# Kernel tuning notes

Measured on AMD Instinct MI355X. Metric: run time of the kernel, lower is better.

## Reference

```python
import jax, jax.numpy as jnp
import numpy as np

B, LT, LI, DT, DI, D, H = 128, 96, 64, 1024, 2048, 1024, 4
NEG = -2.0 ** 31  # tf.pow(-2.0, 31)
EPS = 1e-3        # keras LayerNormalization default epsilon


def _mha(q_in, k_in, v_in, q_mask, k_mask, Wq, Wk, Wv, Wo):
    # tf split-heads: chunk i of axis 2 -> head i; reshape (B,L,H,d) matches.
    d = D // H
    b = q_in.shape[0]
    q = (q_in @ Wq).reshape(b, -1, H, d)
    k = (k_in @ Wk).reshape(b, -1, H, d)
    v = (v_in @ Wv).reshape(b, -1, H, d)
    scores = jnp.einsum('bqhd,bkhd->bhqk', q, k) / jnp.sqrt(jnp.float32(d))
    mask = (q_mask != 0)[:, None, :, None] & (k_mask != 0)[:, None, None, :]  # [B,1,Lq,Lk]
    scores = jnp.where(mask, scores, NEG)
    attn = jax.nn.softmax(scores, axis=-1)
    attn = jnp.where(mask, attn, 0.0)  # dropout rate is 0.0 -> identity
    out = jnp.einsum('bhqk,bkhd->bqhd', attn, v).reshape(b, -1, D)
    return out @ Wo


def _ln(x, g, b):
    m = jnp.mean(x, axis=-1, keepdims=True)
    v = jnp.var(x, axis=-1, keepdims=True)
    return (x - m) / jnp.sqrt(v + EPS) * g + b


def setup_inputs() -> dict:
    key = jax.random.key(0)
    ks = iter(jax.random.split(key, 40))
    s = 0.02
    inp = {
        'text_embedding': jax.random.normal(next(ks), (B, LT, DT), jnp.float32),
        'image_embedding': jax.random.normal(next(ks), (B, LI, DI), jnp.float32),
        'text_mask': jax.random.randint(next(ks), (B, LT), 0, 2, jnp.int32),
        'image_mask': jax.random.randint(next(ks), (B, LI), 0, 2, jnp.int32),
        'W_tp': jax.random.normal(next(ks), (DT, D), jnp.float32) * s,
        'b_tp': jnp.zeros((D,), jnp.float32),
        'W_ip': jax.random.normal(next(ks), (DI, D), jnp.float32) * s,
        'b_ip': jnp.zeros((D,), jnp.float32),
        # text cross-attn (query=image_proj, key=text_proj, value=RAW text)
        'ta_Wq': jax.random.normal(next(ks), (D, D), jnp.float32) * s,
        'ta_Wk': jax.random.normal(next(ks), (D, D), jnp.float32) * s,
        'ta_Wv': jax.random.normal(next(ks), (DT, D), jnp.float32) * s,
        'ta_Wo': jax.random.normal(next(ks), (D, D), jnp.float32) * s,
        # image cross-attn (query=text_proj, key=image_proj, value=RAW image)
        'ia_Wq': jax.random.normal(next(ks), (D, D), jnp.float32) * s,
        'ia_Wk': jax.random.normal(next(ks), (D, D), jnp.float32) * s,
        'ia_Wv': jax.random.normal(next(ks), (DI, D), jnp.float32) * s,
        'ia_Wo': jax.random.normal(next(ks), (D, D), jnp.float32) * s,
        # self-attention blocks
        'ts_Wq': jax.random.normal(next(ks), (D, D), jnp.float32) * s,
        'ts_Wk': jax.random.normal(next(ks), (D, D), jnp.float32) * s,
        'ts_Wv': jax.random.normal(next(ks), (D, D), jnp.float32) * s,
        'ts_Wo': jax.random.normal(next(ks), (D, D), jnp.float32) * s,
        'is_Wq': jax.random.normal(next(ks), (D, D), jnp.float32) * s,
        'is_Wk': jax.random.normal(next(ks), (D, D), jnp.float32) * s,
        'is_Wv': jax.random.normal(next(ks), (D, D), jnp.float32) * s,
        'is_Wo': jax.random.normal(next(ks), (D, D), jnp.float32) * s,
        # layernorm params
        'ln_ta_g': jnp.ones((D,), jnp.float32), 'ln_ta_b': jnp.zeros((D,), jnp.float32),
        'ln_ia_g': jnp.ones((D,), jnp.float32), 'ln_ia_b': jnp.zeros((D,), jnp.float32),
        'ln_ts_g': jnp.ones((D,), jnp.float32), 'ln_ts_b': jnp.zeros((D,), jnp.float32),
        'ln_is_g': jnp.ones((D,), jnp.float32), 'ln_is_b': jnp.zeros((D,), jnp.float32),
    }
    return inp


def reference(text_embedding, image_embedding, text_mask, image_mask,
              W_tp, b_tp, W_ip, b_ip,
              ta_Wq, ta_Wk, ta_Wv, ta_Wo,
              ia_Wq, ia_Wk, ia_Wv, ia_Wo,
              ts_Wq, ts_Wk, ts_Wv, ts_Wo,
              is_Wq, is_Wk, is_Wv, is_Wo,
              ln_ta_g, ln_ta_b, ln_ia_g, ln_ia_b,
              ln_ts_g, ln_ts_b, ln_is_g, ln_is_b):
    text_proj = text_embedding @ W_tp + b_tp    # [B,LT,D]
    image_proj = image_embedding @ W_ip + b_ip  # [B,LI,D]
    # cross attention (note asymmetric query/key masks, raw-value inputs)
    text_att = _mha(image_proj, text_proj, text_embedding, image_mask, text_mask,
                    ta_Wq, ta_Wk, ta_Wv, ta_Wo)   # [B,LI,D]
    image_att = _mha(text_proj, image_proj, image_embedding, text_mask, image_mask,
                     ia_Wq, ia_Wk, ia_Wv, ia_Wo)  # [B,LT,D]
    text_att = _ln(text_att, ln_ta_g, ln_ta_b)
    image_att = _ln(image_att, ln_ia_g, ln_ia_b)
    # self attention
    text_att = _mha(text_att, text_att, text_att, image_mask, image_mask,
                    ts_Wq, ts_Wk, ts_Wv, ts_Wo)
    image_att = _mha(image_att, image_att, image_att, text_mask, text_mask,
                     is_Wq, is_Wk, is_Wv, is_Wo)
    text_att = _ln(text_att, ln_ts_g, ln_ts_b)
    image_att = _ln(image_att, ln_is_g, ln_is_b)
    return (text_att, image_att)
```

## Files before the change

### kernel.cpp

```cpp
#include <hip/hip_runtime.h>

typedef __bf16 bf16_t;
typedef __attribute__((ext_vector_type(8))) __bf16 bf16x8;
typedef __attribute__((ext_vector_type(4))) __bf16 bf16x4;
typedef __attribute__((ext_vector_type(4))) float f32x4;

__device__ __forceinline__ void async_copy16(const bf16_t* g, bf16_t* l) {
    __builtin_amdgcn_global_load_lds(
        (const __attribute__((address_space(1))) void*)g,
        (__attribute__((address_space(3))) void*)l, 16, 0, 0);
}

__global__ __launch_bounds__(256) void transpose_to_bf16(const float* __restrict__ in,
                                                         bf16_t* __restrict__ out,
                                                         int K, int N) {
    __shared__ float tile[32][33];
    int t = threadIdx.x;
    int tx = t & 31, ty = t >> 5;
    int n0 = blockIdx.x * 32, k0 = blockIdx.y * 32;
#pragma unroll
    for (int i = 0; i < 4; i++) {
        int k = k0 + ty + i * 8;
        tile[ty + i * 8][tx] = in[(size_t)k * N + n0 + tx];
    }
    __syncthreads();
#pragma unroll
    for (int i = 0; i < 4; i++) {
        int n = n0 + ty + i * 8;
        out[(size_t)n * K + k0 + tx] = (bf16_t)tile[tx][ty + i * 8];
    }
}

__global__ __launch_bounds__(256) void gemm_bt(const bf16_t* __restrict__ A,
                                               const bf16_t* __restrict__ Bt,
                                               const float* __restrict__ bias,
                                               float* __restrict__ outF,
                                               bf16_t* __restrict__ outB,
                                               int M, int N, int K) {
    __shared__ bf16_t As[128 * 32];
    __shared__ bf16_t Bs[128 * 32];
    const int t = threadIdx.x;
    const int w = t >> 6, lane = t & 63;
    const int quad = lane >> 4, l16 = lane & 15;
    const int bm = blockIdx.x * 128, bn = blockIdx.y * 128;
    const int wm = (w >> 1) * 64, wn = (w & 1) * 64;

    const f32x4 zero = {0.f, 0.f, 0.f, 0.f};
    f32x4 acc[4][4];
#pragma unroll
    for (int i = 0; i < 4; i++)
#pragma unroll
        for (int j = 0; j < 4; j++) acc[i][j] = zero;

    const int srow = t >> 2;
    const int scol = (t & 3) * 8;
    const bf16_t* ga = A + (size_t)(bm + srow) * K + scol;
    const bf16_t* gb = Bt + (size_t)(bn + srow) * K + scol;
    bf16_t* la = As + w * 512;
    bf16_t* lb = Bs + w * 512;

    for (int k0 = 0; k0 < K; k0 += 32) {
        async_copy16(ga + k0, la);
        async_copy16(ga + k0 + (size_t)64 * K, la + 2048);
        async_copy16(gb + k0, lb);
        async_copy16(gb + k0 + (size_t)64 * K, lb + 2048);
        __syncthreads();
        bf16x8 af[4], bf[4];
#pragma unroll
        for (int i = 0; i < 4; i++)
            af[i] = *(const bf16x8*)(As + (wm + i * 16 + l16) * 32 + quad * 8);
#pragma unroll
        for (int j = 0; j < 4; j++)
            bf[j] = *(const bf16x8*)(Bs + (wn + j * 16 + l16) * 32 + quad * 8);
#pragma unroll
        for (int i = 0; i < 4; i++)
#pragma unroll
            for (int j = 0; j < 4; j++)
                acc[i][j] = __builtin_amdgcn_mfma_f32_16x16x32_bf16(af[i], bf[j], acc[i][j], 0, 0, 0);
        __syncthreads();
    }

#pragma unroll
    for (int i = 0; i < 4; i++) {
        int r0 = bm + wm + i * 16 + quad * 4;
#pragma unroll
        for (int j = 0; j < 4; j++) {
            int c = bn + wn + j * 16 + l16;
            float bsv = bias ? bias[c] : 0.f;
#pragma unroll
            for (int r = 0; r < 4; r++) {
                float v = acc[i][j][r] + bsv;
                size_t idx = (size_t)(r0 + r) * N + c;
                if (outF) outF[idx] = v;
                if (outB) outB[idx] = (bf16_t)v;
            }
        }
    }
}

__global__ __launch_bounds__(256) void gemm_f32a(const float* __restrict__ A,
                                                 const bf16_t* __restrict__ Bt,
                                                 const float* __restrict__ bias,
                                                 bf16_t* __restrict__ outB,
                                                 int M, int N, int K) {
    __shared__ bf16_t As[128 * 32];
    __shared__ bf16_t Bs[128 * 32];
    const int t = threadIdx.x;
    const int w = t >> 6, lane = t & 63;
    const int quad = lane >> 4, l16 = lane & 15;
    const int bm = blockIdx.x * 128, bn = blockIdx.y * 128;
    const int wm = (w >> 1) * 64, wn = (w & 1) * 64;

    const f32x4 zero = {0.f, 0.f, 0.f, 0.f};
    f32x4 acc[4][4];
#pragma unroll
    for (int i = 0; i < 4; i++)
#pragma unroll
        for (int j = 0; j < 4; j++) acc[i][j] = zero;

    const int arow = t >> 1, acol = (t & 1) * 16;
    const float* ga = A + (size_t)(bm + arow) * K + acol;
    const int srow = t >> 2, scol = (t & 3) * 8;
    const bf16_t* gb = Bt + (size_t)(bn + srow) * K + scol;
    bf16_t* lb = Bs + w * 512;

    for (int k0 = 0; k0 < K; k0 += 32) {
        async_copy16(gb + k0, lb);
        async_copy16(gb + k0 + (size_t)64 * K, lb + 2048);
        float4 v0 = *(const float4*)(ga + k0);
        float4 v1 = *(const float4*)(ga + k0 + 4);
        float4 v2 = *(const float4*)(ga + k0 + 8);
        float4 v3 = *(const float4*)(ga + k0 + 12);
        bf16x8 o0, o1;
        o0[0] = (__bf16)v0.x; o0[1] = (__bf16)v0.y; o0[2] = (__bf16)v0.z; o0[3] = (__bf16)v0.w;
        o0[4] = (__bf16)v1.x; o0[5] = (__bf16)v1.y; o0[6] = (__bf16)v1.z; o0[7] = (__bf16)v1.w;
        o1[0] = (__bf16)v2.x; o1[1] = (__bf16)v2.y; o1[2] = (__bf16)v2.z; o1[3] = (__bf16)v2.w;
        o1[4] = (__bf16)v3.x; o1[5] = (__bf16)v3.y; o1[6] = (__bf16)v3.z; o1[7] = (__bf16)v3.w;
        *(bf16x8*)(As + arow * 32 + acol) = o0;
        *(bf16x8*)(As + arow * 32 + acol + 8) = o1;
        __syncthreads();
        bf16x8 af[4], bf[4];
#pragma unroll
        for (int i = 0; i < 4; i++)
            af[i] = *(const bf16x8*)(As + (wm + i * 16 + l16) * 32 + quad * 8);
#pragma unroll
        for (int j = 0; j < 4; j++)
            bf[j] = *(const bf16x8*)(Bs + (wn + j * 16 + l16) * 32 + quad * 8);
#pragma unroll
        for (int i = 0; i < 4; i++)
#pragma unroll
            for (int j = 0; j < 4; j++)
                acc[i][j] = __builtin_amdgcn_mfma_f32_16x16x32_bf16(af[i], bf[j], acc[i][j], 0, 0, 0);
        __syncthreads();
    }

#pragma unroll
    for (int i = 0; i < 4; i++) {
        int r0 = bm + wm + i * 16 + quad * 4;
#pragma unroll
        for (int j = 0; j < 4; j++) {
            int c = bn + wn + j * 16 + l16;
            float bsv = bias ? bias[c] : 0.f;
#pragma unroll
            for (int r = 0; r < 4; r++)
                outB[(size_t)(r0 + r) * N + c] = (bf16_t)(acc[i][j][r] + bsv);
        }
    }
}

template <int LQ, int LK>
__global__ __launch_bounds__(256) void attn_kernel(const bf16_t* __restrict__ Q,
                                                   const bf16_t* __restrict__ Kb,
                                                   const bf16_t* __restrict__ V,
                                                   const int* __restrict__ qmask,
                                                   const int* __restrict__ kmask,
                                                   bf16_t* __restrict__ O) {
    constexpr int VSTR = LK + 8;
    constexpr int NQT = LQ / 16, NKT = LK / 16, NKB = LK / 32;
    __shared__ bf16_t Vt[256 * VSTR];
    __shared__ bf16_t Pb[4 * 16 * LK];

    const int t = threadIdx.x;
    const int w = t >> 6, lane = t & 63;
    const int quad = lane >> 4, l16 = lane & 15;
    const int b = blockIdx.x >> 2;
    const int h = blockIdx.x & 3;
    const int hoff = h * 256;

    for (int idx = t; idx < LK * 32; idx += 256) {
        int k = idx % LK;
        int e0 = (idx / LK) * 8;
        bf16x8 v = *(const bf16x8*)(V + (size_t)(b * LK + k) * 1024 + hoff + e0);
#pragma unroll
        for (int j = 0; j < 8; j++) Vt[(e0 + j) * VSTR + k] = v[j];
    }
    __syncthreads();

    bf16_t* P = Pb + w * (16 * LK);

    for (int qt = w; qt < NQT; qt += 4) {
        const int qrow = b * LQ + qt * 16;
        bf16x8 qf[8];
#pragma unroll
        for (int kb = 0; kb < 8; kb++)
            qf[kb] = *(const bf16x8*)(Q + (size_t)(qrow + l16) * 1024 + hoff + kb * 32 + quad * 8);

        f32x4 s[NKT];
        const f32x4 zero = {0.f, 0.f, 0.f, 0.f};
#pragma unroll
        for (int nt = 0; nt < NKT; nt++) {
            f32x4 a = zero;
#pragma unroll
            for (int kb = 0; kb < 8; kb++) {
                bf16x8 kf = *(const bf16x8*)(Kb + (size_t)(b * LK + nt * 16 + l16) * 1024 + hoff + kb * 32 + quad * 8);
                a = __builtin_amdgcn_mfma_f32_16x16x32_bf16(qf[kb], kf, a, 0, 0, 0);
            }
            s[nt] = a;
        }

        int km[NKT];
#pragma unroll
        for (int nt = 0; nt < NKT; nt++) km[nt] = kmask[b * LK + nt * 16 + l16];
        int qmv[4];
#pragma unroll
        for (int r = 0; r < 4; r++) qmv[r] = qmask[b * LQ + qt * 16 + quad * 4 + r];

        float rmax[4], rsum[4];
#pragma unroll
        for (int r = 0; r < 4; r++) rmax[r] = -3.0e38f;
#pragma unroll
        for (int nt = 0; nt < NKT; nt++)
#pragma unroll
            for (int r = 0; r < 4; r++) {
                float v = s[nt][r] * 0.0625f;
                bool ok = (qmv[r] != 0) && (km[nt] != 0);
                s[nt][r] = ok ? v : -3.0e38f;
                rmax[r] = fmaxf(rmax[r], s[nt][r]);
            }
#pragma unroll
        for (int r = 0; r < 4; r++)
            for (int off = 1; off < 16; off <<= 1)
                rmax[r] = fmaxf(rmax[r], __shfl_xor(rmax[r], off, 16));
#pragma unroll
        for (int r = 0; r < 4; r++) rsum[r] = 0.f;
#pragma unroll
        for (int nt = 0; nt < NKT; nt++)
#pragma unroll
            for (int r = 0; r < 4; r++) {
                float p = (s[nt][r] > -1.0e38f) ? __expf(s[nt][r] - rmax[r]) : 0.f;
                s[nt][r] = p;
                rsum[r] += p;
            }
#pragma unroll
        for (int r = 0; r < 4; r++)
            for (int off = 1; off < 16; off <<= 1)
                rsum[r] += __shfl_xor(rsum[r], off, 16);
#pragma unroll
        for (int r = 0; r < 4; r++) rsum[r] = (rsum[r] > 0.f) ? 1.f / rsum[r] : 0.f;

#pragma unroll
        for (int nt = 0; nt < NKT; nt++)
#pragma unroll
            for (int r = 0; r < 4; r++)
                P[(quad * 4 + r) * LK + nt * 16 + l16] = (bf16_t)(s[nt][r] * rsum[r]);
        asm volatile("s_waitcnt lgkmcnt(0)" ::: "memory");

        bf16x8 pf[NKB];
#pragma unroll
        for (int kb = 0; kb < NKB; kb++)
            pf[kb] = *(const bf16x8*)(P + l16 * LK + kb * 32 + quad * 8);

#pragma unroll
        for (int et = 0; et < 16; et++) {
            f32x4 o = zero;
#pragma unroll
            for (int kb = 0; kb < NKB; kb++) {
                bf16x8 vf = *(const bf16x8*)(Vt + (et * 16 + l16) * VSTR + kb * 32 + quad * 8);
                o = __builtin_amdgcn_mfma_f32_16x16x32_bf16(pf[kb], vf, o, 0, 0, 0);
            }
#pragma unroll
            for (int r = 0; r < 4; r++)
                O[(size_t)(qrow + quad * 4 + r) * 1024 + hoff + et * 16 + l16] = (bf16_t)o[r];
        }
    }
}

__global__ __launch_bounds__(256) void ln_kernel(const float* __restrict__ in,
                                                 const float* __restrict__ g,
                                                 const float* __restrict__ be,
                                                 float* __restrict__ outF,
                                                 bf16_t* __restrict__ outB) {
    __shared__ float red[8];
    const int row = blockIdx.x, t = threadIdx.x;
    const float* x = in + (size_t)row * 1024;
    float4 v = *(const float4*)(x + t * 4);
    float s = v.x + v.y + v.z + v.w;
    float ss = v.x * v.x + v.y * v.y + v.z * v.z + v.w * v.w;
    for (int off = 1; off < 64; off <<= 1) {
        s += __shfl_xor(s, off);
        ss += __shfl_xor(ss, off);
    }
    int w = t >> 6, lane = t & 63;
    if (lane == 0) { red[w * 2] = s; red[w * 2 + 1] = ss; }
    __syncthreads();
    if (t == 0) {
        float a = 0.f, b2 = 0.f;
        for (int i = 0; i < 4; i++) { a += red[i * 2]; b2 += red[i * 2 + 1]; }
        red[0] = a; red[1] = b2;
    }
    __syncthreads();
    float mean = red[0] * (1.f / 1024.f);
    float var = red[1] * (1.f / 1024.f) - mean * mean;
    float rstd = rsqrtf(var + 1e-3f);
    float4 gv = *(const float4*)(g + t * 4);
    float4 bv = *(const float4*)(be + t * 4);
    float y0 = (v.x - mean) * rstd * gv.x + bv.x;
    float y1 = (v.y - mean) * rstd * gv.y + bv.y;
    float y2 = (v.z - mean) * rstd * gv.z + bv.z;
    float y3 = (v.w - mean) * rstd * gv.w + bv.w;
    if (outF) {
        float4 o = {y0, y1, y2, y3};
        *(float4*)(outF + (size_t)row * 1024 + t * 4) = o;
    }
    if (outB) {
        bf16x4 o;
        o[0] = (__bf16)y0; o[1] = (__bf16)y1; o[2] = (__bf16)y2; o[3] = (__bf16)y3;
        *(bf16x4*)(outB + (size_t)row * 1024 + t * 4) = o;
    }
}

extern "C" void kernel_launch(void* const* d_in, const int* in_sizes, int n_in,
                              void* d_out, int out_size, void* d_ws, size_t ws_size,
                              hipStream_t stream) {
    (void)in_sizes; (void)n_in; (void)out_size; (void)ws_size;
    const float* tE = (const float*)d_in[0];
    const float* iE = (const float*)d_in[1];
    const int* tMask = (const int*)d_in[2];
    const int* iMask = (const int*)d_in[3];

    char* ws = (char*)d_ws;
    const size_t SLOT = (size_t)12288 * 1024 * 2;
    bf16_t* S[6];
    for (int i = 0; i < 6; i++) S[i] = (bf16_t*)(ws + i * SLOT);
    bf16_t* Wb = (bf16_t*)(ws + 6 * SLOT);
    float* f32_01 = (float*)S[0];
    float* f32_23 = (float*)S[2];

    auto TW = [&](int idx) {
        int K = (idx == 6 || idx == 14) ? 2048 : 1024;
        transpose_to_bf16<<<dim3(32, K / 32), 256, 0, stream>>>((const float*)d_in[idx], Wb, K, 1024);
    };
    auto gemm = [&](const bf16_t* A, const float* bias, float* oF, bf16_t* oB, int M, int K) {
        gemm_bt<<<dim3(M / 128, 8), 256, 0, stream>>>(A, Wb, bias, oF, oB, M, 1024, K);
    };
    auto gemmF = [&](const float* A, const float* bias, bf16_t* oB, int M, int K) {
        gemm_f32a<<<dim3(M / 128, 8), 256, 0, stream>>>(A, Wb, bias, oB, M, 1024, K);
    };

    TW(4);  gemmF(tE, (const float*)d_in[5], S[0], 12288, 1024);
    TW(6);  gemmF(iE, (const float*)d_in[7], S[1], 8192, 2048);
    TW(8);  gemm(S[1], nullptr, nullptr, S[2], 8192, 1024);
    TW(9);  gemm(S[0], nullptr, nullptr, S[3], 12288, 1024);
    TW(10); gemmF(tE, nullptr, S[4], 12288, 1024);
    attn_kernel<64, 96><<<512, 256, 0, stream>>>(S[2], S[3], S[4], iMask, tMask, S[5]);
    TW(12); gemm(S[0], nullptr, nullptr, S[2], 12288, 1024);
    TW(13); gemm(S[1], nullptr, nullptr, S[3], 8192, 1024);
    TW(14); gemmF(iE, nullptr, S[4], 8192, 2048);
    attn_kernel<96, 64><<<512, 256, 0, stream>>>(S[2], S[3], S[4], tMask, iMask, S[0]);
    TW(11); gemm(S[5], nullptr, f32_23, nullptr, 8192, 1024);
    ln_kernel<<<8192, 256, 0, stream>>>(f32_23, (const float*)d_in[24], (const float*)d_in[25], nullptr, S[1]);
    TW(15); gemm(S[0], nullptr, f32_23, nullptr, 12288, 1024);
    ln_kernel<<<12288, 256, 0, stream>>>(f32_23, (const float*)d_in[26], (const float*)d_in[27], nullptr, S[4]);
    TW(16); gemm(S[1], nullptr, nullptr, S[0], 8192, 1024);
    TW(17); gemm(S[1], nullptr, nullptr, S[2], 8192, 1024);
    TW(18); gemm(S[1], nullptr, nullptr, S[3], 8192, 1024);
    attn_kernel<64, 64><<<512, 256, 0, stream>>>(S[0], S[2], S[3], iMask, iMask, S[5]);
    TW(19); gemm(S[5], nullptr, f32_01, nullptr, 8192, 1024);
    ln_kernel<<<8192, 256, 0, stream>>>(f32_01, (const float*)d_in[28], (const float*)d_in[29], (float*)d_out, nullptr);
    TW(20); gemm(S[4], nullptr, nullptr, S[2], 12288, 1024);
    TW(21); gemm(S[4], nullptr, nullptr, S[3], 12288, 1024);
    TW(22); gemm(S[4], nullptr, nullptr, S[5], 12288, 1024);
    attn_kernel<96, 96><<<512, 256, 0, stream>>>(S[2], S[3], S[5], tMask, tMask, S[0]);
    TW(23); gemm(S[0], nullptr, f32_23, nullptr, 12288, 1024);
    ln_kernel<<<12288, 256, 0, stream>>>(f32_23, (const float*)d_in[30], (const float*)d_in[31],
                                         (float*)d_out + 8388608, nullptr);
}
```

Baseline: 1.184 ms.

## Batch projection GEMMs sharing an input into wide multi-output launches

Projections that read the same activation are merged into one GEMM with a wider N, via grouped weight transposes and a multi-pointer epilogue. This covers text proj with its value projection, image proj with its value projection, the Q/K pairs and the fused self-attention QKV. The f32-input GEMM now loads A with a row-strided pattern into padded LDS to reduce bank conflicts. Output-projection results are written as bf16 instead of f32, which halves LN input traffic but adds rounding before the layer norm. The intent is fewer launches, better GPU fill, and fewer passes over the shared activations.

Measured after the change: 1.076 ms. 9.1% less time.

```diff
diff --git a/kernel.cpp b/kernel.cpp
--- a/kernel.cpp
+++ b/kernel.cpp
@@ -11,9 +11,15 @@
         (__attribute__((address_space(3))) void*)l, 16, 0, 0);
 }
 
-__global__ __launch_bounds__(256) void transpose_to_bf16(const float* __restrict__ in,
-                                                         bf16_t* __restrict__ out,
-                                                         int K, int N) {
+__global__ __launch_bounds__(256) void transpose_group(const float* __restrict__ s0,
+                                                       const float* __restrict__ s1,
+                                                       const float* __restrict__ s2,
+                                                       bf16_t* __restrict__ dst, int K) {
+    const float* in;
+    if (blockIdx.z == 0) in = s0;
+    else if (blockIdx.z == 1) in = s1;
+    else in = s2;
+    bf16_t* out = dst + (size_t)blockIdx.z * 1024 * K;
     __shared__ float tile[32][33];
     int t = threadIdx.x;
     int tx = t & 31, ty = t >> 5;
@@ -21,7 +27,7 @@
 #pragma unroll
     for (int i = 0; i < 4; i++) {
         int k = k0 + ty + i * 8;
-        tile[ty + i * 8][tx] = in[(size_t)k * N + n0 + tx];
+        tile[ty + i * 8][tx] = in[(size_t)k * 1024 + n0 + tx];
     }
     __syncthreads();
 #pragma unroll
@@ -31,11 +37,18 @@
     }
 }
 
+__global__ __launch_bounds__(256) void fuse_bias(const float* __restrict__ src,
+                                                 float* __restrict__ out) {
+    int i = blockIdx.x * 256 + threadIdx.x;
+    out[i] = (i < 1024) ? src[i] : 0.f;
+}
+
 __global__ __launch_bounds__(256) void gemm_bt(const bf16_t* __restrict__ A,
                                                const bf16_t* __restrict__ Bt,
                                                const float* __restrict__ bias,
-                                               float* __restrict__ outF,
-                                               bf16_t* __restrict__ outB,
+                                               bf16_t* __restrict__ o0,
+                                               bf16_t* __restrict__ o1,
+                                               bf16_t* __restrict__ o2,
                                                int M, int N, int K) {
     __shared__ bf16_t As[128 * 32];
     __shared__ bf16_t Bs[128 * 32];
@@ -80,20 +93,22 @@
         __syncthreads();
     }
 
+    bf16_t* out;
+    if (bn < 1024) out = o0;
+    else if (bn < 2048) out = o1;
+    else out = o2;
+    const int cb = bn & 1023;
+    const int bbase = bn - cb;
 #pragma unroll
     for (int i = 0; i < 4; i++) {
         int r0 = bm + wm + i * 16 + quad * 4;
 #pragma unroll
         for (int j = 0; j < 4; j++) {
-            int c = bn + wn + j * 16 + l16;
-            float bsv = bias ? bias[c] : 0.f;
-#pragma unroll
-            for (int r = 0; r < 4; r++) {
-                float v = acc[i][j][r] + bsv;
-                size_t idx = (size_t)(r0 + r) * N + c;
-                if (outF) outF[idx] = v;
-                if (outB) outB[idx] = (bf16_t)v;
-            }
+            int c = cb + wn + j * 16 + l16;
+            float bsv = bias ? bias[bbase + c] : 0.f;
+#pragma unroll
+            for (int r = 0; r < 4; r++)
+                out[(size_t)(r0 + r) * 1024 + c] = (bf16_t)(acc[i][j][r] + bsv);
         }
     }
 }
@@ -101,9 +116,11 @@
 __global__ __launch_bounds__(256) void gemm_f32a(const float* __restrict__ A,
                                                  const bf16_t* __restrict__ Bt,
                                                  const float* __restrict__ bias,
-                                                 bf16_t* __restrict__ outB,
+                                                 bf16_t* __restrict__ o0,
+                                                 bf16_t* __restrict__ o1,
                                                  int M, int N, int K) {
-    __shared__ bf16_t As[128 * 32];
+    constexpr int ASTR = 40;
+    __shared__ bf16_t As[128 * ASTR];
     __shared__ bf16_t Bs[128 * 32];
     const int t = threadIdx.x;
     const int w = t >> 6, lane = t & 63;
@@ -118,8 +135,8 @@
 #pragma unroll
         for (int j = 0; j < 4; j++) acc[i][j] = zero;
 
-    const int arow = t >> 1, acol = (t & 1) * 16;
-    const float* ga = A + (size_t)(bm + arow) * K + acol;
+    const int arow = t >> 3, ac4 = (t & 7) * 4;
+    const float* ga = A + (size_t)(bm + arow) * K + ac4;
     const int srow = t >> 2, scol = (t & 3) * 8;
     const bf16_t* gb = Bt + (size_t)(bn + srow) * K + scol;
     bf16_t* lb = Bs + w * 512;
@@ -127,22 +144,22 @@
     for (int k0 = 0; k0 < K; k0 += 32) {
         async_copy16(gb + k0, lb);
         async_copy16(gb + k0 + (size_t)64 * K, lb + 2048);
-        float4 v0 = *(const float4*)(ga + k0);
-        float4 v1 = *(const float4*)(ga + k0 + 4);
-        float4 v2 = *(const float4*)(ga + k0 + 8);
-        float4 v3 = *(const float4*)(ga + k0 + 12);
-        bf16x8 o0, o1;
-        o0[0] = (__bf16)v0.x; o0[1] = (__bf16)v0.y; o0[2] = (__bf16)v0.z; o0[3] = (__bf16)v0.w;
-        o0[4] = (__bf16)v1.x; o0[5] = (__bf16)v1.y; o0[6] = (__bf16)v1.z; o0[7] = (__bf16)v1.w;
-        o1[0] = (__bf16)v2.x; o1[1] = (__bf16)v2.y; o1[2] = (__bf16)v2.z; o1[3] = (__bf16)v2.w;
-        o1[4] = (__bf16)v3.x; o1[5] = (__bf16)v3.y; o1[6] = (__bf16)v3.z; o1[7] = (__bf16)v3.w;
-        *(bf16x8*)(As + arow * 32 + acol) = o0;
-        *(bf16x8*)(As + arow * 32 + acol + 8) = o1;
+        float4 av[4];
+#pragma unroll
+        for (int i = 0; i < 4; i++)
+            av[i] = *(const float4*)(ga + (size_t)i * 32 * K + k0);
+#pragma unroll
+        for (int i = 0; i < 4; i++) {
+            bf16x4 c;
+            c[0] = (__bf16)av[i].x; c[1] = (__bf16)av[i].y;
+            c[2] = (__bf16)av[i].z; c[3] = (__bf16)av[i].w;
+            *(bf16x4*)(As + (arow + i * 32) * ASTR + ac4) = c;
+        }
         __syncthreads();
         bf16x8 af[4], bf[4];
 #pragma unroll
         for (int i = 0; i < 4; i++)
-            af[i] = *(const bf16x8*)(As + (wm + i * 16 + l16) * 32 + quad * 8);
+            af[i] = *(const bf16x8*)(As + (wm + i * 16 + l16) * ASTR + quad * 8);
 #pragma unroll
         for (int j = 0; j < 4; j++)
             bf[j] = *(const bf16x8*)(Bs + (wn + j * 16 + l16) * 32 + quad * 8);
@@ -154,16 +171,19 @@
         __syncthreads();
     }
 
+    bf16_t* out = (bn < 1024) ? o0 : o1;
+    const int cb = bn & 1023;
+    const int bbase = bn - cb;
 #pragma unroll
     for (int i = 0; i < 4; i++) {
         int r0 = bm + wm + i * 16 + quad * 4;
 #pragma unroll
         for (int j = 0; j < 4; j++) {
-            int c = bn + wn + j * 16 + l16;
-            float bsv = bias ? bias[c] : 0.f;
+            int c = cb + wn + j * 16 + l16;
+            float bsv = bias ? bias[bbase + c] : 0.f;
 #pragma unroll
             for (int r = 0; r < 4; r++)
-                outB[(size_t)(r0 + r) * N + c] = (bf16_t)(acc[i][j][r] + bsv);
+                out[(size_t)(r0 + r) * 1024 + c] = (bf16_t)(acc[i][j][r] + bsv);
         }
     }
 }
@@ -285,17 +305,17 @@
     }
 }
 
-__global__ __launch_bounds__(256) void ln_kernel(const float* __restrict__ in,
+__global__ __launch_bounds__(256) void ln_kernel(const bf16_t* __restrict__ in,
                                                  const float* __restrict__ g,
                                                  const float* __restrict__ be,
                                                  float* __restrict__ outF,
                                                  bf16_t* __restrict__ outB) {
     __shared__ float red[8];
     const int row = blockIdx.x, t = threadIdx.x;
-    const float* x = in + (size_t)row * 1024;
-    float4 v = *(const float4*)(x + t * 4);
-    float s = v.x + v.y + v.z + v.w;
-    float ss = v.x * v.x + v.y * v.y + v.z * v.z + v.w * v.w;
+    bf16x4 xb = *(const bf16x4*)(in + (size_t)row * 1024 + t * 4);
+    float x0 = (float)xb[0], x1 = (float)xb[1], x2 = (float)xb[2], x3 = (float)xb[3];
+    float s = x0 + x1 + x2 + x3;
+    float ss = x0 * x0 + x1 * x1 + x2 * x2 + x3 * x3;
     for (int off = 1; off < 64; off <<= 1) {
         s += __shfl_xor(s, off);
         ss += __shfl_xor(ss, off);
@@ -314,10 +334,10 @@
     float rstd = rsqrtf(var + 1e-3f);
     float4 gv = *(const float4*)(g + t * 4);
     float4 bv = *(const float4*)(be + t * 4);
-    float y0 = (v.x - mean) * rstd * gv.x + bv.x;
-    float y1 = (v.y - mean) * rstd * gv.y + bv.y;
-    float y2 = (v.z - mean) * rstd * gv.z + bv.z;
-    float y3 = (v.w - mean) * rstd * gv.w + bv.w;
+    float y0 = (x0 - mean) * rstd * gv.x + bv.x;
+    float y1 = (x1 - mean) * rstd * gv.y + bv.y;
+    float y2 = (x2 - mean) * rstd * gv.z + bv.z;
+    float y3 = (x3 - mean) * rstd * gv.w + bv.w;
     if (outF) {
         float4 o = {y0, y1, y2, y3};
         *(float4*)(outF + (size_t)row * 1024 + t * 4) = o;
@@ -338,50 +358,54 @@
     const int* tMask = (const int*)d_in[2];
     const int* iMask = (const int*)d_in[3];
 
+    const size_t MB = 1048576;
     char* ws = (char*)d_ws;
-    const size_t SLOT = (size_t)12288 * 1024 * 2;
-    bf16_t* S[6];
-    for (int i = 0; i < 6; i++) S[i] = (bf16_t*)(ws + i * SLOT);
-    bf16_t* Wb = (bf16_t*)(ws + 6 * SLOT);
-    float* f32_01 = (float*)S[0];
-    float* f32_23 = (float*)S[2];
-
-    auto TW = [&](int idx) {
-        int K = (idx == 6 || idx == 14) ? 2048 : 1024;
-        transpose_to_bf16<<<dim3(32, K / 32), 256, 0, stream>>>((const float*)d_in[idx], Wb, K, 1024);
+    bf16_t* WB = (bf16_t*)ws;
+    float* biasT = (float*)(ws + 8 * MB);
+    float* biasI = biasT + 2048;
+    char* AB = ws + 9 * MB;
+    auto buf = [&](int mb) { return (bf16_t*)(AB + (size_t)mb * MB); };
+
+    auto TG = [&](int i0, int i1, int i2, int parts, int K) {
+        transpose_group<<<dim3(32, K / 32, parts), 256, 0, stream>>>(
+            (const float*)d_in[i0], i1 >= 0 ? (const float*)d_in[i1] : (const float*)d_in[i0],
+            i2 >= 0 ? (const float*)d_in[i2] : (const float*)d_in[i0], WB, K);
     };
-    auto gemm = [&](const bf16_t* A, const float* bias, float* oF, bf16_t* oB, int M, int K) {
-        gemm_bt<<<dim3(M / 128, 8), 256, 0, stream>>>(A, Wb, bias, oF, oB, M, 1024, K);
+    auto gemm = [&](const bf16_t* A, const float* bias, bf16_t* out0, bf16_t* out1,
+                    bf16_t* out2, int M, int N, int K) {
+        gemm_bt<<<dim3(M / 128, N / 128), 256, 0, stream>>>(A, WB, bias, out0, out1, out2, M, N, K);
     };
-    auto gemmF = [&](const float* A, const float* bias, bf16_t* oB, int M, int K) {
-        gemm_f32a<<<dim3(M / 128, 8), 256, 0, stream>>>(A, Wb, bias, oB, M, 1024, K);
-    };
-
-    TW(4);  gemmF(tE, (const float*)d_in[5], S[0], 12288, 1024);
-    TW(6);  gemmF(iE, (const float*)d_in[7], S[1], 8192, 2048);
-    TW(8);  gemm(S[1], nullptr, nullptr, S[2], 8192, 1024);
-    TW(9);  gemm(S[0], nullptr, nullptr, S[3], 12288, 1024);
-    TW(10); gemmF(tE, nullptr, S[4], 12288, 1024);
-    attn_kernel<64, 96><<<512, 256, 0, stream>>>(S[2], S[3], S[4], iMask, tMask, S[5]);
-    TW(12); gemm(S[0], nullptr, nullptr, S[2], 12288, 1024);
-    TW(13); gemm(S[1], nullptr, nullptr, S[3], 8192, 1024);
-    TW(14); gemmF(iE, nullptr, S[4], 8192, 2048);
-    attn_kernel<96, 64><<<512, 256, 0, stream>>>(S[2], S[3], S[4], tMask, iMask, S[0]);
-    TW(11); gemm(S[5], nullptr, f32_23, nullptr, 8192, 1024);
-    ln_kernel<<<8192, 256, 0, stream>>>(f32_23, (const float*)d_in[24], (const float*)d_in[25], nullptr, S[1]);
-    TW(15); gemm(S[0], nullptr, f32_23, nullptr, 12288, 1024);
-    ln_kernel<<<12288, 256, 0, stream>>>(f32_23, (const float*)d_in[26], (const float*)d_in[27], nullptr, S[4]);
-    TW(16); gemm(S[1], nullptr, nullptr, S[0], 8192, 1024);
-    TW(17); gemm(S[1], nullptr, nullptr, S[2], 8192, 1024);
-    TW(18); gemm(S[1], nullptr, nullptr, S[3], 8192, 1024);
-    attn_kernel<64, 64><<<512, 256, 0, stream>>>(S[0], S[2], S[3], iMask, iMask, S[5]);
-    TW(19); gemm(S[5], nullptr, f32_01, nullptr, 8192, 1024);
-    ln_kernel<<<8192, 256, 0, stream>>>(f32_01, (const float*)d_in[28], (const float*)d_in[29], (float*)d_out, nullptr);
-    TW(20); gemm(S[4], nullptr, nullptr, S[2], 12288, 1024);
-    TW(21); gemm(S[4], nullptr, nullptr, S[3], 12288, 1024);
-    TW(22); gemm(S[4], nullptr, nullptr, S[5], 12288, 1024);
-    attn_kernel<96, 96><<<512, 256, 0, stream>>>(S[2], S[3], S[5], tMask, tMask, S[0]);
-    TW(23); gemm(S[0], nullptr, f32_23, nullptr, 12288, 1024);
-    ln_kernel<<<12288, 256, 0, stream>>>(f32_23, (const float*)d_in[30], (const float*)d_in[31],
+
+    fuse_bias<<<8, 256, 0, stream>>>((const float*)d_in[5], biasT);
+    fuse_bias<<<8, 256, 0, stream>>>((const float*)d_in[7], biasI);
+
+    TG(4, 10, -1, 2, 1024);
+    gemm_f32a<<<dim3(96, 16), 256, 0, stream>>>(tE, WB, biasT, buf(32), buf(64), 12288, 2048, 1024);
+    TG(6, 14, -1, 2, 2048);
+    gemm_f32a<<<dim3(64, 16), 256, 0, stream>>>(iE, WB, biasI, buf(0), buf(16), 8192, 2048, 2048);
+    TG(9, 12, -1, 2, 1024);
+    gemm(buf(32), nullptr, buf(88), buf(112), nullptr, 12288, 2048, 1024);
+    TG(8, 13, -1, 2, 1024);
+    gemm(buf(0), nullptr, buf(32), buf(48), nullptr, 8192, 2048, 1024);
+    attn_kernel<64, 96><<<512, 256, 0, stream>>>(buf(32), buf(88), buf(64), iMask, tMask, buf(0));
+    attn_kernel<96, 64><<<512, 256, 0, stream>>>(buf(112), buf(48), buf(16), tMask, iMask, buf(64));
+    TG(11, -1, -1, 1, 1024);
+    gemm(buf(0), nullptr, buf(32), nullptr, nullptr, 8192, 1024, 1024);
+    ln_kernel<<<8192, 256, 0, stream>>>(buf(32), (const float*)d_in[24], (const float*)d_in[25], nullptr, buf(88));
+    TG(15, -1, -1, 1, 1024);
+    gemm(buf(64), nullptr, buf(0), nullptr, nullptr, 12288, 1024, 1024);
+    ln_kernel<<<12288, 256, 0, stream>>>(buf(0), (const float*)d_in[26], (const float*)d_in[27], nullptr, buf(104));
+    TG(16, 17, 18, 3, 1024);
+    gemm(buf(88), nullptr, buf(0), buf(16), buf(32), 8192, 3072, 1024);
+    attn_kernel<64, 64><<<512, 256, 0, stream>>>(buf(0), buf(16), buf(32), iMask, iMask, buf(48));
+    TG(19, -1, -1, 1, 1024);
+    gemm(buf(48), nullptr, buf(64), nullptr, nullptr, 8192, 1024, 1024);
+    ln_kernel<<<8192, 256, 0, stream>>>(buf(64), (const float*)d_in[28], (const float*)d_in[29], (float*)d_out, nullptr);
+    TG(20, 21, 22, 3, 1024);
+    gemm(buf(104), nullptr, buf(0), buf(24), buf(48), 12288, 3072, 1024);
+    attn_kernel<96, 96><<<512, 256, 0, stream>>>(buf(0), buf(24), buf(48), tMask, tMask, buf(72));
+    TG(23, -1, -1, 1, 1024);
+    gemm(buf(72), nullptr, buf(96), nullptr, nullptr, 12288, 1024, 1024);
+    ln_kernel<<<12288, 256, 0, stream>>>(buf(96), (const float*)d_in[30], (const float*)d_in[31],
                                          (float*)d_out + 8388608, nullptr);
 }
```
